# Kernel optimization log

Hardware: AMD Instinct MI355X
Metric: run time of the kernel (lower is better)

## Reference

```python
import jax, jax.numpy as jnp
import numpy as np

R = 31                 # max_radius
K = 2 * R + 1          # kernel length = 63
SIGMA_RATIO = 1.6
STIMULUS_SCALE = 1.0
CPS_HALF = 1.0
EPS = 1e-3             # gauss_epsilon

B, C, H, W = 4, 32, 512, 512


def setup_inputs() -> dict:
    key = jax.random.key(0)
    k1, k2 = jax.random.split(key)
    x = jax.random.normal(k1, (B, C, H, W), dtype=jnp.float32)
    # positive per-pixel sigma map in a realistic range
    sigma_map = jax.random.uniform(k2, (B, H, W), dtype=jnp.float32,
                                   minval=0.5, maxval=8.0)
    return {"x": x, "sigma_map": sigma_map}


def _gauss_weights(sigma):
    """sigma: [B,H,W] -> normalized truncated-Gaussian weights [B,K,H,W]."""
    r = jnp.arange(-R, R + 1, dtype=jnp.float32).reshape(1, K, 1, 1)
    G = jnp.exp(-0.5 * (r / sigma[:, None]) ** 2)          # [B,K,H,W]
    G = G * (G >= EPS)                                      # hard truncation
    return G / (G.sum(axis=1, keepdims=True) + 1e-8)


def _sep_blur(x, G):
    """Separable spatially-varying blur. x: [B,C,H,W], G: [B,K,H,W].
    Instead of materializing the [B,C,K,H,W] unfold tensor (as the torch
    code does), accumulate the K shifted slices with a fixed-length scan —
    identical math, O(K) less peak memory."""
    def pass1d(x_pad, axis, length):
        def body(acc, k):
            sl = jax.lax.dynamic_slice_in_dim(x_pad, k, length, axis=axis)  # [B,C,H,W]
            g = jax.lax.dynamic_index_in_dim(G, k, axis=1, keepdims=False)  # [B,H,W]
            return acc + sl * g[:, None], None
        acc0 = jnp.zeros(x.shape, x.dtype)
        out, _ = jax.lax.scan(body, acc0, jnp.arange(K))
        return out

    # horizontal pass (pad W by R with reflect, as F.pad(..., mode='reflect'))
    x_pad = jnp.pad(x, ((0, 0), (0, 0), (0, 0), (R, R)), mode='reflect')
    out_h = pass1d(x_pad, axis=3, length=x.shape[3])
    # vertical pass (pad H by R)
    out_pad = jnp.pad(out_h, ((0, 0), (0, 0), (R, R), (0, 0)), mode='reflect')
    return pass1d(out_pad, axis=2, length=x.shape[2])


def reference(x, sigma_map):
    sigma1 = sigma_map * STIMULUS_SCALE / CPS_HALF
    G1 = _gauss_weights(sigma1)
    G2 = _gauss_weights(sigma1 * SIGMA_RATIO)
    out1 = _sep_blur(x, G1)
    out2 = _sep_blur(x, G2)
    return out2 - out1
```

## Files before the change

kernel.cpp:

```cpp
#include <hip/hip_runtime.h>
#include <stdint.h>

typedef unsigned short u16;
typedef unsigned int   u32;

#define RR 31
#define WW 512
#define HH 512
#define BB 4
#define CC 32
#define EPSW 1e-3f

__device__ __forceinline__ int reflect512(int i) {
    i = (i < 0) ? -i : i;
    return (i >= WW) ? (2*WW - 2 - i) : i;
}

__device__ __forceinline__ u16 f2bf(float f) {
    u32 u = __float_as_uint(f);
    u32 r = (u + 0x7fffu + ((u >> 16) & 1u)) >> 16;
    return (u16)r;
}

__device__ __forceinline__ void unpack4(uint2 v, float* o) {
    union { u32 u; float f; } a, b, c, d;
    a.u = v.x << 16; b.u = v.x & 0xffff0000u;
    c.u = v.y << 16; d.u = v.y & 0xffff0000u;
    o[0] = a.f; o[1] = b.f; o[2] = c.f; o[3] = d.f;
}

__global__ __launch_bounds__(256, 4)
void hpass(const float* __restrict__ x, const float* __restrict__ sig,
           u32* __restrict__ ws)
{
    __shared__ float xs[4][576];
    const int t  = threadIdx.x;
    const int c0 = blockIdx.x * 4;
    const int h  = blockIdx.y;
    const int b  = blockIdx.z;

    #pragma unroll
    for (int c = 0; c < 4; ++c) {
        const float* src = x + ((size_t)((b*CC + c0 + c)*HH + h))*WW;
        for (int i = t; i < 576; i += 256)
            xs[c][i] = src[reflect512(i - 32)];
    }
    __syncthreads();

    const int w0 = t * 2;
    float2 sg = *(const float2*)(sig + ((size_t)(b*HH + h))*WW + w0);

    float m1[2], q1[2], wv1[2], S1[2], m2[2], q2[2], wv2[2], S2[2];
    #pragma unroll
    for (int p = 0; p < 2; ++p) {
        float s   = p ? sg.y : sg.x;
        float tt1 = -0.5f / (s*s);
        m1[p] = __expf(tt1);             q1[p] = m1[p]*m1[p];
        float tt2 = tt1 * (1.0f/2.56f);
        m2[p] = __expf(tt2);             q2[p] = m2[p]*m2[p];
        wv1[p] = 1.f; wv2[p] = 1.f; S1[p] = 0.f; S2[p] = 0.f;
    }

    float a1[4][2], a2[4][2];
    float2 Lhi[4], Rlo[4];
    #pragma unroll
    for (int c = 0; c < 4; ++c) {
        float2 Cq = *(const float2*)&xs[c][32 + w0];
        a1[c][0] = Cq.x; a1[c][1] = Cq.y;
        a2[c][0] = Cq.x; a2[c][1] = Cq.y;
        Lhi[c] = Cq; Rlo[c] = Cq;
    }

    #pragma unroll 1
    for (int kb = 0; kb < 15; ++kb) {
        float tw1[2][2], tw2[2][2];
        #pragma unroll
        for (int j = 0; j < 2; ++j)
            #pragma unroll
            for (int p = 0; p < 2; ++p) {
                wv1[p] *= m1[p]; m1[p] *= q1[p];
                float ta = (wv1[p] >= EPSW) ? wv1[p] : 0.f;
                tw1[j][p] = ta; S1[p] += ta;
                wv2[p] *= m2[p]; m2[p] *= q2[p];
                float tb = (wv2[p] >= EPSW) ? wv2[p] : 0.f;
                tw2[j][p] = tb; S2[p] += tb;
            }
        const int li = 32 + w0 - 2 - 2*kb;
        const int ri = 32 + w0 + 2 + 2*kb;
        #pragma unroll
        for (int c = 0; c < 4; ++c) {
            float2 Llo = *(const float2*)&xs[c][li];
            float2 Rhi = *(const float2*)&xs[c][ri];
            float s00 = Llo.y    + Rlo[c].y;
            float s01 = Llo.x    + Rhi.x;
            float s10 = Lhi[c].x + Rhi.x;
            float s11 = Llo.y    + Rhi.y;
            a1[c][0] = fmaf(tw1[0][0], s00, a1[c][0]);
            a1[c][0] = fmaf(tw1[1][0], s01, a1[c][0]);
            a1[c][1] = fmaf(tw1[0][1], s10, a1[c][1]);
            a1[c][1] = fmaf(tw1[1][1], s11, a1[c][1]);
            a2[c][0] = fmaf(tw2[0][0], s00, a2[c][0]);
            a2[c][0] = fmaf(tw2[1][0], s01, a2[c][0]);
            a2[c][1] = fmaf(tw2[0][1], s10, a2[c][1]);
            a2[c][1] = fmaf(tw2[1][1], s11, a2[c][1]);
            Lhi[c] = Llo; Rlo[c] = Rhi;
        }
    }

    {
        float t1e[2], t2e[2];
        #pragma unroll
        for (int p = 0; p < 2; ++p) {
            wv1[p] *= m1[p];
            float ta = (wv1[p] >= EPSW) ? wv1[p] : 0.f;
            t1e[p] = ta; S1[p] += ta;
            wv2[p] *= m2[p];
            float tb = (wv2[p] >= EPSW) ? wv2[p] : 0.f;
            t2e[p] = tb; S2[p] += tb;
        }
        const int li = 32 + w0 - 32;
        const int ri = 32 + w0 + 32;
        #pragma unroll
        for (int c = 0; c < 4; ++c) {
            float2 Lle = *(const float2*)&xs[c][li];
            float2 Rre = *(const float2*)&xs[c][ri];
            float s0 = Lle.y    + Rlo[c].y;
            float s1 = Lhi[c].x + Rre.x;
            a1[c][0] = fmaf(t1e[0], s0, a1[c][0]);
            a1[c][1] = fmaf(t1e[1], s1, a1[c][1]);
            a2[c][0] = fmaf(t2e[0], s0, a2[c][0]);
            a2[c][1] = fmaf(t2e[1], s1, a2[c][1]);
        }
    }

    float n1[2], n2[2];
    #pragma unroll
    for (int p = 0; p < 2; ++p) {
        n1[p] = 1.0f / (1.0f + 2.0f*S1[p] + 1e-8f);
        n2[p] = 1.0f / (1.0f + 2.0f*S2[p] + 1e-8f);
    }
    #pragma unroll
    for (int c = 0; c < 4; ++c) {
        uint2 pk;
        pk.x = (u32)f2bf(a1[c][0]*n1[0]) | ((u32)f2bf(a2[c][0]*n2[0]) << 16);
        pk.y = (u32)f2bf(a1[c][1]*n1[1]) | ((u32)f2bf(a2[c][1]*n2[1]) << 16);
        size_t base = ((size_t)((b*CC + c0 + c)*HH + h))*WW + w0;
        *(uint2*)(ws + base) = pk;
    }
}

__global__ __launch_bounds__(1024, 4)
void vpass(const u32* __restrict__ ws, const float* __restrict__ sig,
           float* __restrict__ out)
{
    __shared__ __align__(16) u16 ls[2][4*32*32*4];
    const int t   = threadIdx.x;
    const int w   = t & 31;
    const int hq  = (t >> 5) & 15;
    const int g   = t >> 9;
    const int wg0 = blockIdx.x * 32;
    const int h0  = blockIdx.y * 64;
    const int bz  = blockIdx.z;
    const int b   = bz >> 3;
    const int c0  = (bz & 7) * 4;

    #pragma unroll
    for (int c = 0; c < 4; ++c) {
        const u32* src = ws + ((size_t)((b*CC + c0 + c)*HH))*WW;
        #pragma unroll
        for (int it = 0; it < 4; ++it) {
            int idx = t + it*1024;
            int r = idx >> 5, wl = idx & 31;
            int hh = reflect512(h0 - 32 + r);
            u32 v = src[hh*WW + wg0 + wl];
            int li = ((c*32 + wl) << 7) + (((r >> 2) ^ (wl & 15)) << 2) + (r & 3);
            ls[0][li] = (u16)v;
            ls[1][li] = (u16)(v >> 16);
        }
    }
    __syncthreads();

    float mm[4], qq[4], wv[4], S[4];
    #pragma unroll
    for (int p = 0; p < 4; ++p) {
        float s  = sig[((size_t)(b*HH + h0 + 4*hq + p))*WW + wg0 + w];
        float tt = -0.5f / (s*s);
        if (g) tt *= (1.0f/2.56f);
        mm[p] = __expf(tt); qq[p] = mm[p]*mm[p];
        wv[p] = 1.f; S[p] = 0.f;
    }

    const u16* lg = &ls[g][0];
    float a[4][4];
    uint2 CL[4], CR[4];
    const int qc = 8 + hq;
    #pragma unroll
    for (int c = 0; c < 4; ++c) {
        uint2 v = *(const uint2*)&lg[((c*32 + w) << 7) + ((qc ^ (w & 15)) << 2)];
        float f[4]; unpack4(v, f);
        #pragma unroll
        for (int p = 0; p < 4; ++p) a[c][p] = f[p];
        CL[c] = v; CR[c] = v;
    }

    #pragma unroll 1
    for (int kb = 0; kb < 8; ++kb) {
        float tw[4][4];
        #pragma unroll
        for (int j = 0; j < 4; ++j)
            #pragma unroll
            for (int p = 0; p < 4; ++p) {
                wv[p] *= mm[p]; mm[p] *= qq[p];
                float ta = (wv[p] >= EPSW) ? wv[p] : 0.f;
                if (j == 3) ta = (kb == 7) ? 0.f : ta;
                tw[j][p] = ta; S[p] += ta;
            }
        const int ql = 7 + hq - kb;
        const int qr = 9 + hq + kb;
        #pragma unroll
        for (int c = 0; c < 4; ++c) {
            const int rowb = (c*32 + w) << 7;
            uint2 Lq = *(const uint2*)&lg[rowb + ((ql ^ (w & 15)) << 2)];
            uint2 Rq = *(const uint2*)&lg[rowb + ((qr ^ (w & 15)) << 2)];
            float lv[8], rv[8];
            unpack4(Lq, &lv[0]);    unpack4(CL[c], &lv[4]);
            unpack4(CR[c], &rv[0]); unpack4(Rq, &rv[4]);
            #pragma unroll
            for (int j = 0; j < 4; ++j)
                #pragma unroll
                for (int p = 0; p < 4; ++p) {
                    float s = lv[p - j + 3] + rv[p + j + 1];
                    a[c][p] = fmaf(tw[j][p], s, a[c][p]);
                }
            CL[c] = Lq; CR[c] = Rq;
        }
    }

    float n[4];
    #pragma unroll
    for (int p = 0; p < 4; ++p) n[p] = 1.0f / (1.0f + 2.0f*S[p] + 1e-8f);

    __syncthreads();
    float* xch = (float*)&ls[0][0];
    if (g == 0) {
        #pragma unroll
        for (int c = 0; c < 4; ++c)
            #pragma unroll
            for (int p = 0; p < 4; ++p)
                xch[((c*16 + hq)*4 + p)*32 + w] = a[c][p]*n[p];
    }
    __syncthreads();
    if (g == 1) {
        #pragma unroll
        for (int c = 0; c < 4; ++c)
            #pragma unroll
            for (int p = 0; p < 4; ++p) {
                size_t o = ((size_t)((b*CC + c0 + c)*HH + h0 + 4*hq + p))*WW + wg0 + w;
                out[o] = a[c][p]*n[p] - xch[((c*16 + hq)*4 + p)*32 + w];
            }
    }
}

extern "C" void kernel_launch(void* const* d_in, const int* in_sizes, int n_in,
                              void* d_out, int out_size, void* d_ws, size_t ws_size,
                              hipStream_t stream) {
    const float* x   = (const float*)d_in[0];
    const float* sig = (const float*)d_in[1];
    float* out = (float*)d_out;

    const size_t n = (size_t)BB*CC*HH*WW;
    if (ws_size < n * sizeof(u32)) return;
    u32* ws = (u32*)d_ws;

    hpass<<<dim3(8, 512, 4), 256, 0, stream>>>(x, sig, ws);
    vpass<<<dim3(16, 8, 32), 1024, 0, stream>>>(ws, sig, out);
}
```

Baseline: 434.8 us.

## Recast vertical blur as banded bf16 MFMA matmul with channel-last workspace

The horizontal pass now writes its bf16 intermediate channel-innermost, as [B,H,W,C]. The vertical pass then treats the 63-tap spatially-varying blur as a banded matrix product: per-output-row Gaussian weights are built as MFMA B fragments and multiplied against channel×row tiles with mfma_f32_16x16x32_bf16. This replaces the scalar FMA loops with matrix cores. The cost is recomputing exp-weights per fragment, including zero-padded band entries, plus a transpose through LDS to write NCHW output. The per-row normalization sums are precomputed with a 31-term exp loop.

```diff
diff --git a/kernel.cpp b/kernel.cpp
--- a/kernel.cpp
+++ b/kernel.cpp
@@ -4,13 +4,17 @@
 typedef unsigned short u16;
 typedef unsigned int   u32;
 
-#define RR 31
 #define WW 512
 #define HH 512
 #define BB 4
 #define CC 32
 #define EPSW 1e-3f
 
+typedef __bf16 bf16x8 __attribute__((ext_vector_type(8)));
+typedef short  s16x8  __attribute__((ext_vector_type(8)));
+
+union FragU { s16x8 s; bf16x8 b; };
+
 __device__ __forceinline__ int reflect512(int i) {
     i = (i < 0) ? -i : i;
     return (i >= WW) ? (2*WW - 2 - i) : i;
@@ -20,13 +24,6 @@
     u32 u = __float_as_uint(f);
     u32 r = (u + 0x7fffu + ((u >> 16) & 1u)) >> 16;
     return (u16)r;
-}
-
-__device__ __forceinline__ void unpack4(uint2 v, float* o) {
-    union { u32 u; float f; } a, b, c, d;
-    a.u = v.x << 16; b.u = v.x & 0xffff0000u;
-    c.u = v.y << 16; d.u = v.y & 0xffff0000u;
-    o[0] = a.f; o[1] = b.f; o[2] = c.f; o[3] = d.f;
 }
 
 __global__ __launch_bounds__(256, 4)
@@ -56,7 +53,7 @@
         float s   = p ? sg.y : sg.x;
         float tt1 = -0.5f / (s*s);
         m1[p] = __expf(tt1);             q1[p] = m1[p]*m1[p];
-        float tt2 = tt1 * (1.0f/2.56f);
+        float tt2 = tt1 * 0.390625f;
         m2[p] = __expf(tt2);             q2[p] = m2[p]*m2[p];
         wv1[p] = 1.f; wv2[p] = 1.f; S1[p] = 0.f; S2[p] = 0.f;
     }
@@ -140,124 +137,149 @@
         n2[p] = 1.0f / (1.0f + 2.0f*S2[p] + 1e-8f);
     }
     #pragma unroll
-    for (int c = 0; c < 4; ++c) {
-        uint2 pk;
-        pk.x = (u32)f2bf(a1[c][0]*n1[0]) | ((u32)f2bf(a2[c][0]*n2[0]) << 16);
-        pk.y = (u32)f2bf(a1[c][1]*n1[1]) | ((u32)f2bf(a2[c][1]*n2[1]) << 16);
-        size_t base = ((size_t)((b*CC + c0 + c)*HH + h))*WW + w0;
-        *(uint2*)(ws + base) = pk;
-    }
-}
-
-__global__ __launch_bounds__(1024, 4)
+    for (int p = 0; p < 2; ++p) {
+        uint4 pk;
+        u32* pq = (u32*)&pk;
+        #pragma unroll
+        for (int c = 0; c < 4; ++c)
+            pq[c] = (u32)f2bf(a1[c][p]*n1[p]) | ((u32)f2bf(a2[c][p]*n2[p]) << 16);
+        size_t idx = ((size_t)(b*HH + h)*WW + (w0 + p))*CC + c0;
+        *(uint4*)(ws + idx) = pk;
+    }
+}
+
+__global__ __launch_bounds__(512)
 void vpass(const u32* __restrict__ ws, const float* __restrict__ sig,
            float* __restrict__ out)
 {
-    __shared__ __align__(16) u16 ls[2][4*32*32*4];
-    const int t   = threadIdx.x;
-    const int w   = t & 31;
-    const int hq  = (t >> 5) & 15;
-    const int g   = t >> 9;
-    const int wg0 = blockIdx.x * 32;
-    const int h0  = blockIdx.y * 64;
-    const int bz  = blockIdx.z;
-    const int b   = bz >> 3;
-    const int c0  = (bz & 7) * 4;
-
-    #pragma unroll
-    for (int c = 0; c < 4; ++c) {
-        const u32* src = ws + ((size_t)((b*CC + c0 + c)*HH))*WW;
-        #pragma unroll
-        for (int it = 0; it < 4; ++it) {
-            int idx = t + it*1024;
-            int r = idx >> 5, wl = idx & 31;
-            int hh = reflect512(h0 - 32 + r);
-            u32 v = src[hh*WW + wg0 + wl];
-            int li = ((c*32 + wl) << 7) + (((r >> 2) ^ (wl & 15)) << 2) + (r & 3);
-            ls[0][li] = (u16)v;
-            ls[1][li] = (u16)(v >> 16);
-        }
-    }
-    __syncthreads();
-
-    float mm[4], qq[4], wv[4], S[4];
-    #pragma unroll
-    for (int p = 0; p < 4; ++p) {
-        float s  = sig[((size_t)(b*HH + h0 + 4*hq + p))*WW + wg0 + w];
+    __shared__ __align__(16) u16 Ag[8*32*128];
+    __shared__ float tt_l[2*8*64];
+    __shared__ float si_l[2*8*64];
+
+    const int t    = threadIdx.x;
+    const int lane = t & 63;
+    const int wid  = t >> 6;
+    const int w0   = blockIdx.x * 8;
+    const int h0   = blockIdx.y * 64;
+    const int b    = blockIdx.z;
+
+    #pragma unroll
+    for (int i = 0; i < 2; ++i) {
+        int id = t + i*512;
+        int wl = id & 7, h = (id >> 3) & 63, g = id >> 9;
+        float s = sig[(size_t)(b*HH + h0 + h)*WW + w0 + wl];
         float tt = -0.5f / (s*s);
-        if (g) tt *= (1.0f/2.56f);
-        mm[p] = __expf(tt); qq[p] = mm[p]*mm[p];
-        wv[p] = 1.f; S[p] = 0.f;
-    }
-
-    const u16* lg = &ls[g][0];
-    float a[4][4];
-    uint2 CL[4], CR[4];
-    const int qc = 8 + hq;
-    #pragma unroll
-    for (int c = 0; c < 4; ++c) {
-        uint2 v = *(const uint2*)&lg[((c*32 + w) << 7) + ((qc ^ (w & 15)) << 2)];
-        float f[4]; unpack4(v, f);
-        #pragma unroll
-        for (int p = 0; p < 4; ++p) a[c][p] = f[p];
-        CL[c] = v; CR[c] = v;
-    }
+        if (g) tt *= 0.390625f;
+        float S = 0.f;
+        for (int k = 1; k <= 31; ++k) {
+            float wf = __expf(tt * (float)(k*k));
+            S += (wf >= EPSW) ? wf : 0.f;
+        }
+        tt_l[(g*8 + wl)*64 + h] = tt;
+        si_l[(g*8 + wl)*64 + h] = 1.f / (1.f + 2.f*S + 1e-8f);
+    }
+
+    float acc0[4][2][4], acc1[4][2][4];
 
     #pragma unroll 1
-    for (int kb = 0; kb < 8; ++kb) {
-        float tw[4][4];
-        #pragma unroll
-        for (int j = 0; j < 4; ++j)
-            #pragma unroll
-            for (int p = 0; p < 4; ++p) {
-                wv[p] *= mm[p]; mm[p] *= qq[p];
-                float ta = (wv[p] >= EPSW) ? wv[p] : 0.f;
-                if (j == 3) ta = (kb == 7) ? 0.f : ta;
-                tw[j][p] = ta; S[p] += ta;
-            }
-        const int ql = 7 + hq - kb;
-        const int qr = 9 + hq + kb;
-        #pragma unroll
-        for (int c = 0; c < 4; ++c) {
-            const int rowb = (c*32 + w) << 7;
-            uint2 Lq = *(const uint2*)&lg[rowb + ((ql ^ (w & 15)) << 2)];
-            uint2 Rq = *(const uint2*)&lg[rowb + ((qr ^ (w & 15)) << 2)];
-            float lv[8], rv[8];
-            unpack4(Lq, &lv[0]);    unpack4(CL[c], &lv[4]);
-            unpack4(CR[c], &rv[0]); unpack4(Rq, &rv[4]);
-            #pragma unroll
-            for (int j = 0; j < 4; ++j)
+    for (int g = 0; g < 2; ++g) {
+        __syncthreads();
+        {
+            const int c   = t & 31;
+            const int grp = t >> 5;
+            #pragma unroll
+            for (int w8 = 0; w8 < 8; ++w8)
                 #pragma unroll
-                for (int p = 0; p < 4; ++p) {
-                    float s = lv[p - j + 3] + rv[p + j + 1];
-                    a[c][p] = fmaf(tw[j][p], s, a[c][p]);
+                for (int rp = 0; rp < 4; ++rp) {
+                    int r0  = (rp*16 + grp)*2;
+                    int hh0 = reflect512(h0 - 32 + r0);
+                    int hh1 = reflect512(h0 - 31 + r0);
+                    u32 v0 = ws[((size_t)(b*HH + hh0)*WW + w0 + w8)*CC + c];
+                    u32 v1 = ws[((size_t)(b*HH + hh1)*WW + w0 + w8)*CC + c];
+                    u32 lo0 = g ? (v0 >> 16) : (v0 & 0xffffu);
+                    u32 lo1 = g ? (v1 >> 16) : (v1 & 0xffffu);
+                    int idx = ((w8*32 + c) << 7) + ((((r0 >> 3) ^ (c & 15))) << 3) + (r0 & 7);
+                    *(u32*)&Ag[idx] = lo0 | (lo1 << 16);
                 }
-            CL[c] = Lq; CR[c] = Rq;
-        }
-    }
-
-    float n[4];
-    #pragma unroll
-    for (int p = 0; p < 4; ++p) n[p] = 1.0f / (1.0f + 2.0f*S[p] + 1e-8f);
-
-    __syncthreads();
-    float* xch = (float*)&ls[0][0];
-    if (g == 0) {
-        #pragma unroll
-        for (int c = 0; c < 4; ++c)
-            #pragma unroll
-            for (int p = 0; p < 4; ++p)
-                xch[((c*16 + hq)*4 + p)*32 + w] = a[c][p]*n[p];
-    }
-    __syncthreads();
-    if (g == 1) {
-        #pragma unroll
-        for (int c = 0; c < 4; ++c)
-            #pragma unroll
-            for (int p = 0; p < 4; ++p) {
-                size_t o = ((size_t)((b*CC + c0 + c)*HH + h0 + 4*hq + p))*WW + wg0 + w;
-                out[o] = a[c][p]*n[p] - xch[((c*16 + hq)*4 + p)*32 + w];
-            }
+        }
+        __syncthreads();
+
+        FragU af[2][4];
+        #pragma unroll
+        for (int ch = 0; ch < 2; ++ch)
+            #pragma unroll
+            for (int kt = 0; kt < 4; ++kt) {
+                int cc   = ch*16 + (lane & 15);
+                int gran = kt*4 + (lane >> 4);
+                int idx  = ((wid*32 + cc) << 7) + ((gran ^ (cc & 15)) << 3);
+                af[ch][kt].s = *(const s16x8*)&Ag[idx];
+            }
+
+        #pragma unroll
+        for (int ht = 0; ht < 4; ++ht) {
+            const int h_loc = ht*16 + (lane & 15);
+            const float tt = tt_l[(g*8 + wid)*64 + h_loc];
+            const int kbase = (ht < 2) ? 0 : 1;
+            FragU bfr[3];
+            #pragma unroll
+            for (int kk = 0; kk < 3; ++kk) {
+                int d0 = (kbase + kk)*32 + ((lane >> 4)*8) - h_loc - 32;
+                #pragma unroll
+                for (int j = 0; j < 8; ++j) {
+                    int d = d0 + j;
+                    float fd = (float)d;
+                    float wf = __expf(tt * fd * fd);
+                    bool ok = ((unsigned)(d + 31) <= 62u) && (wf >= EPSW);
+                    float val = ok ? wf : 0.f;
+                    bfr[kk].s[j] = (short)f2bf(val);
+                }
+            }
+            float4 aL = make_float4(0.f, 0.f, 0.f, 0.f);
+            float4 aH = make_float4(0.f, 0.f, 0.f, 0.f);
+            typedef float f32x4 __attribute__((ext_vector_type(4)));
+            f32x4 vL = {0.f,0.f,0.f,0.f}, vH = {0.f,0.f,0.f,0.f};
+            #pragma unroll
+            for (int kk = 0; kk < 3; ++kk) {
+                vL = __builtin_amdgcn_mfma_f32_16x16x32_bf16(af[0][kbase+kk].b, bfr[kk].b, vL, 0, 0, 0);
+                vH = __builtin_amdgcn_mfma_f32_16x16x32_bf16(af[1][kbase+kk].b, bfr[kk].b, vH, 0, 0, 0);
+            }
+            (void)aL; (void)aH;
+            #pragma unroll
+            for (int r = 0; r < 4; ++r) {
+                if (g == 0) { acc0[ht][0][r] = vL[r]; acc0[ht][1][r] = vH[r]; }
+                else        { acc1[ht][0][r] = vL[r]; acc1[ht][1][r] = vH[r]; }
+            }
+        }
+    }
+
+    float* Dl = (float*)Ag;
+    #pragma unroll
+    for (int ch = 0; ch < 2; ++ch) {
+        __syncthreads();
+        #pragma unroll
+        for (int ht = 0; ht < 4; ++ht) {
+            const int h_loc = ht*16 + (lane & 15);
+            float s0 = si_l[(0*8 + wid)*64 + h_loc];
+            float s1 = si_l[(1*8 + wid)*64 + h_loc];
+            #pragma unroll
+            for (int r = 0; r < 4; ++r) {
+                int c_loc = (lane >> 4)*4 + r;
+                float v = acc1[ht][ch][r]*s1 - acc0[ht][ch][r]*s0;
+                Dl[c_loc*576 + h_loc*9 + wid] = v;
+            }
+        }
+        __syncthreads();
+        #pragma unroll
+        for (int r2 = 0; r2 < 2; ++r2) {
+            int rid = t + r2*512;
+            int c_loc = rid >> 6, h = rid & 63;
+            float q[8];
+            #pragma unroll
+            for (int j = 0; j < 8; ++j) q[j] = Dl[c_loc*576 + h*9 + j];
+            size_t gb = ((size_t)((b*CC + ch*16 + c_loc)*HH) + h0 + h)*WW + w0;
+            *(float4*)(out + gb)     = make_float4(q[0], q[1], q[2], q[3]);
+            *(float4*)(out + gb + 4) = make_float4(q[4], q[5], q[6], q[7]);
+        }
     }
 }
 
@@ -273,5 +295,5 @@
     u32* ws = (u32*)d_ws;
 
     hpass<<<dim3(8, 512, 4), 256, 0, stream>>>(x, sig, ws);
-    vpass<<<dim3(16, 8, 32), 1024, 0, stream>>>(ws, sig, out);
-}
+    vpass<<<dim3(64, 8, 4), 512, 0, stream>>>(ws, sig, out);
+}
```

Result: slower. 629.8 us (+44.9%).
